# Performance work log

Measured on AMD Instinct MI355X. Metric: run time of the kernel, lower is better.

Reference implementation:

```python
import jax, jax.numpy as jnp
import numpy as np

B, T, D, NH = 2, 2048, 1024, 16


def setup_inputs() -> dict:
    key = jax.random.key(0)
    ks = jax.random.split(key, 9)
    s = 0.02
    return {
        "x": jax.random.normal(ks[0], (B, T, D), jnp.float32),
        "Wq": jax.random.normal(ks[1], (D, D), jnp.float32) * s,
        "bq": jax.random.normal(ks[2], (D,), jnp.float32) * s,
        "Wk": jax.random.normal(ks[3], (D, D), jnp.float32) * s,
        "bk": jax.random.normal(ks[4], (D,), jnp.float32) * s,
        "Wv": jax.random.normal(ks[5], (D, D), jnp.float32) * s,
        "bv": jax.random.normal(ks[6], (D,), jnp.float32) * s,
        "Wp": jax.random.normal(ks[7], (D, D), jnp.float32) * s,
        "bp": jax.random.normal(ks[8], (D,), jnp.float32) * s,
        "num_heads": NH,
    }


def _alibi_slopes(nh):
    # standard ALiBi slopes: 2^(-8*h/nh), h = 1..nh
    return jnp.asarray(2.0 ** (-8.0 * np.arange(1, nh + 1) / nh), jnp.float32)


def reference(x, Wq, bq, Wk, bk, Wv, bv, Wp, bp, num_heads):
    b, t, k = x.shape
    nh = num_heads
    hd = k // nh
    scale = k ** 0.25  # each of q,k divided by k**0.25 -> scores / sqrt(k)

    def split_heads(y):  # [b,t,k] -> [b,nh,t,hd]
        return y.reshape(b, t, nh, hd).transpose(0, 2, 1, 3)

    q = split_heads(x @ Wq.T + bq) / scale
    kk = split_heads(x @ Wk.T + bk) / scale
    v = split_heads(x @ Wv.T + bv)

    scores = jnp.einsum("bhid,bhjd->bhij", q, kk)  # [b,nh,t,t]

    pos = jnp.arange(t)
    rel = pos[None, :] - pos[:, None]  # j - i, <= 0 on causal side
    slopes = _alibi_slopes(nh)
    scores = scores + slopes[None, :, None, None] * rel[None, None, :, :]

    causal = rel <= 0  # [t,t]
    scores = jnp.where(causal[None, None, :, :], scores, -jnp.inf)

    attn = jax.nn.softmax(scores, axis=-1)
    out = jnp.einsum("bhij,bhjd->bhid", attn, v)  # [b,nh,t,hd]
    out = out.transpose(0, 2, 1, 3).reshape(b, t, k)
    return out @ Wp.T + bp
```

## Files before the change

kernel.cpp:

```cpp
#include <hip/hip_runtime.h>


using f32x4  = __attribute__((ext_vector_type(4))) float;
using bf16x8 = __attribute__((ext_vector_type(8))) short;
typedef unsigned short u16;
using u16x4 = __attribute__((ext_vector_type(4))) u16;
using u32x4 = __attribute__((ext_vector_type(4))) unsigned int;

#define T_SEQ  2048
#define NHEAD  16
#define HDIM   64
#define DMODEL 1024
#define MROWS  4096

#define LOG2E 1.4426950408889634f

__device__ __forceinline__ u16 f2bf(float f) {
  union { float f; unsigned u; } v; v.f = f;
  return (u16)((v.u + 0x7fffu + ((v.u >> 16) & 1u)) >> 16);
}

__device__ __forceinline__ unsigned cvt_pk_bf16(float lo, float hi) {
  unsigned r;
  asm("v_cvt_pk_bf16_f32 %0, %1, %2" : "=v"(r) : "v"(lo), "v"(hi));
  return r;
}

__device__ __forceinline__ void gl_lds16(const u16* g, u16* l) {
  __builtin_amdgcn_global_load_lds(
      (const __attribute__((address_space(1))) unsigned int*)g,
      (__attribute__((address_space(3))) unsigned int*)l, 16, 0, 0);
}

__global__ __launch_bounds__(256) void cvt_bf16(const float* __restrict__ src,
                                                u16* __restrict__ dst, int n) {
  int i = (blockIdx.x * 256 + threadIdx.x) * 4;
  if (i < n) {
    const float4 v = *reinterpret_cast<const float4*>(src + i);
    u16x4 o;
    o.x = f2bf(v.x); o.y = f2bf(v.y); o.z = f2bf(v.z); o.w = f2bf(v.w);
    *reinterpret_cast<u16x4*>(dst + i) = o;
  }
}

__global__ __launch_bounds__(256) void cvt_w4(
    const float* __restrict__ w0, const float* __restrict__ w1,
    const float* __restrict__ w2, const float* __restrict__ w3,
    u16* __restrict__ dst) {
  const float* src = (blockIdx.y == 0) ? w0 : (blockIdx.y == 1) ? w1
                   : (blockIdx.y == 2) ? w2 : w3;
  u16* d = dst + (size_t)blockIdx.y * 1048576;
  int i = (blockIdx.x * 256 + threadIdx.x) * 4;
  const float4 v = *reinterpret_cast<const float4*>(src + i);
  u16x4 o;
  o.x = f2bf(v.x); o.y = f2bf(v.y); o.z = f2bf(v.z); o.w = f2bf(v.w);
  *reinterpret_cast<u16x4*>(d + i) = o;
}

__global__ __launch_bounds__(256, 3) void qkv_gemm(
    const u16* __restrict__ xb,
    const u16* __restrict__ wq, const u16* __restrict__ wk, const u16* __restrict__ wv,
    const float* __restrict__ bq, const float* __restrict__ bk, const float* __restrict__ bv,
    u16* __restrict__ q_ws, u16* __restrict__ k_ws, u16* __restrict__ vt_ws)
{
  const int K = DMODEL;
  const int z = blockIdx.z;
  const u16*   W    = (z == 0) ? wq : (z == 1) ? wk : wv;
  const float* bias = (z == 0) ? bq : (z == 1) ? bk : bv;
  const int bm = blockIdx.y, bn = blockIdx.x;
  const int tid = threadIdx.x;
  const int w = tid >> 6, lane = tid & 63, g = lane >> 4, c = lane & 15;
  const int wm = w >> 1, wn = w & 1;

  __shared__ u16 SM[2][2][128][32];

  f32x4 zero4 = {0.f, 0.f, 0.f, 0.f};
  f32x4 acc[4][4];
#pragma unroll
  for (int m = 0; m < 4; ++m)
#pragma unroll
    for (int n = 0; n < 4; ++n) acc[m][n] = zero4;

  int rr[2], cswz[2];
#pragma unroll
  for (int jj = 0; jj < 2; ++jj) {
    int chunk = tid + 256 * jj;
    rr[jj] = chunk >> 2;
    cswz[jj] = ((chunk & 3) ^ (rr[jj] & 3)) * 8;
  }

  const int fsw = (g ^ (c & 3)) * 8;

#pragma unroll
  for (int jj = 0; jj < 2; ++jj) {
    int chunk = tid + 256 * jj;
    gl_lds16(xb + (size_t)(bm * 128 + rr[jj]) * K + cswz[jj],
             &SM[0][0][0][0] + chunk * 8);
    gl_lds16(W + (size_t)(bn * 128 + rr[jj]) * K + cswz[jj],
             &SM[0][1][0][0] + chunk * 8);
  }
  __syncthreads();

  for (int t = 0; t < 32; ++t) {
    const int buf = t & 1;
    if (t < 31) {
      const int k0 = (t + 1) * 32;
#pragma unroll
      for (int jj = 0; jj < 2; ++jj) {
        int chunk = tid + 256 * jj;
        gl_lds16(xb + (size_t)(bm * 128 + rr[jj]) * K + k0 + cswz[jj],
                 &SM[buf ^ 1][0][0][0] + chunk * 8);
        gl_lds16(W + (size_t)(bn * 128 + rr[jj]) * K + k0 + cswz[jj],
                 &SM[buf ^ 1][1][0][0] + chunk * 8);
      }
    }
    bf16x8 af[4], bfr[4];
#pragma unroll
    for (int m = 0; m < 4; ++m) {
      int row = wm * 64 + m * 16 + c;
      af[m] = *reinterpret_cast<const bf16x8*>(&SM[buf][0][row][fsw]);
    }
#pragma unroll
    for (int n = 0; n < 4; ++n) {
      int row = wn * 64 + n * 16 + c;
      bfr[n] = *reinterpret_cast<const bf16x8*>(&SM[buf][1][row][fsw]);
    }
#pragma unroll
    for (int m = 0; m < 4; ++m)
#pragma unroll
      for (int n = 0; n < 4; ++n)
        acc[m][n] = __builtin_amdgcn_mfma_f32_16x16x32_bf16(af[m], bfr[n], acc[m][n], 0, 0, 0);
    __syncthreads();
  }

  const float rs = 0.1767766953f;
  const float qs = rs * LOG2E;

  if (z == 2) {
    u16* tr = &SM[0][0][0][0];
    const int bb = (bm * 128) >> 11;
    const int t_base = (bm * 128) & (T_SEQ - 1);
#pragma unroll
    for (int hh = 0; hh < 2; ++hh) {
      __syncthreads();
      if (wn == hh) {
#pragma unroll
        for (int n = 0; n < 4; ++n) {
          float bv_ = bias[bn * 128 + wn * 64 + n * 16 + c];
#pragma unroll
          for (int m = 0; m < 4; ++m) {
#pragma unroll
            for (int i = 0; i < 4; ++i) {
              tr[(n * 16 + c) * 136 + wm * 64 + m * 16 + g * 4 + i] =
                  f2bf(acc[m][n][i] + bv_);
            }
          }
        }
      }
      __syncthreads();
#pragma unroll
      for (int rep = 0; rep < 4; ++rep) {
        int idx = tid + rep * 256;
        int dr = idx >> 4, ch = idx & 15;
        bf16x8 vv = *reinterpret_cast<const bf16x8*>(&tr[dr * 136 + ch * 8]);
        int d_glob = bn * 128 + hh * 64 + dr;
        int head = d_glob >> 6, dd = d_glob & 63;
        *reinterpret_cast<bf16x8*>(
            vt_ws + (((size_t)(bb * NHEAD + head) * HDIM + dd) * T_SEQ) + t_base + ch * 8) = vv;
      }
    }
  } else {
    u16* dst = (z == 0) ? q_ws : k_ws;
    const float sc = (z == 0) ? qs : rs;
#pragma unroll
    for (int m = 0; m < 4; ++m) {
      int mrow_base = bm * 128 + wm * 64 + m * 16 + g * 4;
#pragma unroll
      for (int n = 0; n < 4; ++n) {
        int n_idx = bn * 128 + wn * 64 + n * 16 + c;
        float bv_ = bias[n_idx];
        int head = n_idx >> 6, d = n_idx & 63;
#pragma unroll
        for (int i = 0; i < 4; ++i) {
          int mrow = mrow_base + i;
          int b = mrow >> 11, t = mrow & (T_SEQ - 1);
          dst[((size_t)(b * NHEAD + head) * T_SEQ + t) * HDIM + d] =
              f2bf((acc[m][n][i] + bv_) * sc);
        }
      }
    }
  }
}

__global__ __launch_bounds__(128, 2) void attn_fused(
    const u16* __restrict__ Q, const u16* __restrict__ Kk,
    const u16* __restrict__ VT, u16* __restrict__ O)
{
  const int tid = threadIdx.x;
  const int w = tid >> 6;
  const int lane = tid & 63;
  const int g = lane >> 4, c = lane & 15;
  const int c7 = c & 7;
  const int bid = blockIdx.x;
  const int inner = bid >> 3;
  const int bh = (bid & 7) + 8 * (inner & 3);
  const int j = inner >> 2;
  const int h = bh & (NHEAD - 1), b = bh >> 4;
  const float slope2 = exp2f(-0.5f * (float)(h + 1)) * LOG2E;
  const u16* Qp = Q  + (size_t)bh * T_SEQ * HDIM;
  const u16* Kp = Kk + (size_t)bh * T_SEQ * HDIM;
  const u16* Vp = VT + (size_t)bh * HDIM * T_SEQ;

  __shared__ u16 KB[2][64][64];
  __shared__ u16 VB[2][64][64];

  const int s_rb = tid >> 3;
  const int cs = ((tid & 7) ^ (s_rb & 7)) * 8;
  const u16* KsB = Kp + (size_t)s_rb * HDIM + cs;
  const u16* VsB = Vp + (size_t)s_rb * T_SEQ + cs;
  u16* const kd0 = &KB[0][0][0] + tid * 8;
  u16* const vd0 = &VB[0][0][0] + tid * 8;
  const int koffA = c * 64 + ((g ^ c7) * 8);
  const int koffB = c * 64 + (((4 + g) ^ c7) * 8);
  const int vre = c * 64 + (g & 1) * 4;
  const int voff0 = vre + ((((g >> 1) + 0) ^ c7) * 8);
  const int voff1 = vre + ((((g >> 1) + 2) ^ c7) * 8);
  const int voff2 = vre + ((((g >> 1) + 4) ^ c7) * 8);
  const int voff3 = vre + ((((g >> 1) + 6) ^ c7) * 8);

  f32x4 zero4 = {0.f, 0.f, 0.f, 0.f};

  for (int pass = 0; pass < 2; ++pass) {
    const int qb = (pass == 0) ? (63 - j) : j;
    const int q0 = qb * 32;
    const int qrow = q0 + w * 16;
    const int nt = (qb >> 1) + 1;

    bf16x8 qf0 = *reinterpret_cast<const bf16x8*>(Qp + (size_t)(qrow + c) * HDIM + g * 8);
    bf16x8 qf1 = *reinterpret_cast<const bf16x8*>(Qp + (size_t)(qrow + c) * HDIM + 32 + g * 8);

    {
      const int kv0 = (nt - 1) * 64;
      const u16* ks = KsB + kv0 * 64;
      const u16* vs = VsB + kv0;
      gl_lds16(ks,         kd0);
      gl_lds16(ks + 1024,  kd0 + 1024);
      gl_lds16(ks + 2048,  kd0 + 2048);
      gl_lds16(ks + 3072,  kd0 + 3072);
      gl_lds16(vs,          vd0);
      gl_lds16(vs + 32768,  vd0 + 1024);
      gl_lds16(vs + 65536,  vd0 + 2048);
      gl_lds16(vs + 98304,  vd0 + 3072);
    }
    __syncthreads();

    f32x4 o[4];
#pragma unroll
    for (int dg = 0; dg < 4; ++dg) o[dg] = zero4;
    float lrun = 0.f;

    for (int t = 0; t < nt; ++t) {
      const int par = t & 1;
      const u16* kb = &KB[0][0][0] + par * 4096;
      const u16* vb = &VB[0][0][0] + par * 4096;

      if (t + 1 < nt) {
        const int kvn = (nt - 2 - t) * 64;
        const u16* ks = KsB + kvn * 64;
        const u16* vs = VsB + kvn;
        u16* kd = kd0 + (par ^ 1) * 4096;
        u16* vd = vd0 + (par ^ 1) * 4096;
        gl_lds16(ks,         kd);
        gl_lds16(ks + 1024,  kd + 1024);
        gl_lds16(ks + 2048,  kd + 2048);
        gl_lds16(ks + 3072,  kd + 3072);
        gl_lds16(vs,          vd);
        gl_lds16(vs + 32768,  vd + 1024);
        gl_lds16(vs + 65536,  vd + 2048);
        gl_lds16(vs + 98304,  vd + 3072);
      }

      const int kv0 = (nt - 1 - t) * 64;

      const u16* kA = kb + koffA;
      const u16* kBp = kb + koffB;
      f32x4 s[4];
#pragma unroll
      for (int jj = 0; jj < 4; ++jj) {
        bf16x8 k0 = *reinterpret_cast<const bf16x8*>(kA + jj * 1024);
        bf16x8 k1 = *reinterpret_cast<const bf16x8*>(kBp + jj * 1024);
        f32x4 z4 = zero4;
        z4 = __builtin_amdgcn_mfma_f32_16x16x32_bf16(k0, qf0, z4, 0, 0, 0);
        z4 = __builtin_amdgcn_mfma_f32_16x16x32_bf16(k1, qf1, z4, 0, 0, 0);
        s[jj] = z4;
      }

      const int kbase = kv0 + 4 * g - (qrow + c);
      float p[16];
      if (t == 0) {
#pragma unroll
        for (int jj = 0; jj < 4; ++jj)
#pragma unroll
          for (int i = 0; i < 4; ++i) {
            int rel = kbase + 16 * jj + i;
            float sv = s[jj][i] + slope2 * (float)rel;
            if (rel > 0) sv = -3.0e38f;
            float e = __builtin_amdgcn_exp2f(sv);
            p[jj * 4 + i] = e;
            lrun += e;
          }
      } else {
        const float bb2 = slope2 * (float)kbase;
#pragma unroll
        for (int jj = 0; jj < 4; ++jj)
#pragma unroll
          for (int i = 0; i < 4; ++i) {
            float e = __builtin_amdgcn_exp2f(
                s[jj][i] + (bb2 + slope2 * (float)(16 * jj + i)));
            p[jj * 4 + i] = e;
            lrun += e;
          }
      }
      union PU { bf16x8 v; u32x4 u; };
      PU P0, P1;
#pragma unroll
      for (int k = 0; k < 4; ++k) {
        P0.u[k] = cvt_pk_bf16(p[2 * k], p[2 * k + 1]);
        P1.u[k] = cvt_pk_bf16(p[8 + 2 * k], p[8 + 2 * k + 1]);
      }

      const u16* vp0 = vb + voff0;
      const u16* vp1 = vb + voff1;
      const u16* vp2 = vb + voff2;
      const u16* vp3 = vb + voff3;
#pragma unroll
      for (int dg = 0; dg < 4; ++dg) {
        uint2 d0 = *reinterpret_cast<const uint2*>(vp0 + dg * 1024);
        uint2 d1 = *reinterpret_cast<const uint2*>(vp1 + dg * 1024);
        uint2 d2 = *reinterpret_cast<const uint2*>(vp2 + dg * 1024);
        uint2 d3 = *reinterpret_cast<const uint2*>(vp3 + dg * 1024);
        PU vf0, vf1;
        vf0.u[0] = d0.x; vf0.u[1] = d0.y; vf0.u[2] = d1.x; vf0.u[3] = d1.y;
        vf1.u[0] = d2.x; vf1.u[1] = d2.y; vf1.u[2] = d3.x; vf1.u[3] = d3.y;
        o[dg] = __builtin_amdgcn_mfma_f32_16x16x32_bf16(P0.v, vf0.v, o[dg], 0, 0, 0);
        o[dg] = __builtin_amdgcn_mfma_f32_16x16x32_bf16(P1.v, vf1.v, o[dg], 0, 0, 0);
      }

      __syncthreads();
    }

    lrun += __shfl_xor(lrun, 16, 64);
    lrun += __shfl_xor(lrun, 32, 64);
    float rl[4];
#pragma unroll
    for (int i = 0; i < 4; ++i) {
      float li = __shfl(lrun, g * 4 + i, 64);
      rl[i] = 1.0f / li;
    }
#pragma unroll
    for (int dg = 0; dg < 4; ++dg) {
#pragma unroll
      for (int i = 0; i < 4; ++i) {
        int qi = qrow + g * 4 + i;
        O[((size_t)b * T_SEQ + qi) * DMODEL + h * HDIM + dg * 16 + c] =
            f2bf(o[dg][i] * rl[i]);
      }
    }
    __syncthreads();
  }
}

__global__ __launch_bounds__(256) void out_gemm(
    const u16* __restrict__ ao, const u16* __restrict__ wp,
    const float* __restrict__ bp, float* __restrict__ out)
{
  const int K = DMODEL;
  const int bm = blockIdx.y, bn = blockIdx.x;
  const int tid = threadIdx.x;
  const int w = tid >> 6, lane = tid & 63, g = lane >> 4, c = lane & 15;
  const int wm = w >> 1, wn = w & 1;

  __shared__ u16 SM[2][2][128][64];

  f32x4 zero4 = {0.f, 0.f, 0.f, 0.f};
  f32x4 acc[4][4];
#pragma unroll
  for (int m = 0; m < 4; ++m)
#pragma unroll
    for (int n = 0; n < 4; ++n) acc[m][n] = zero4;

  int rr[4], cswz[4];
#pragma unroll
  for (int j = 0; j < 4; ++j) {
    int chunk = tid + 256 * j;
    rr[j] = chunk >> 3;
    cswz[j] = ((chunk & 7) ^ (rr[j] & 7)) * 8;
  }

#pragma unroll
  for (int j = 0; j < 4; ++j) {
    int chunk = tid + 256 * j;
    gl_lds16(ao + (size_t)(bm * 128 + rr[j]) * K + cswz[j],
             &SM[0][0][0][0] + chunk * 8);
    gl_lds16(wp + (size_t)(bn * 128 + rr[j]) * K + cswz[j],
             &SM[0][1][0][0] + chunk * 8);
  }
  __syncthreads();

  for (int t = 0; t < 16; ++t) {
    const int buf = t & 1;
    if (t < 15) {
      const int k0 = (t + 1) * 64;
#pragma unroll
      for (int j = 0; j < 4; ++j) {
        int chunk = tid + 256 * j;
        gl_lds16(ao + (size_t)(bm * 128 + rr[j]) * K + k0 + cswz[j],
                 &SM[buf ^ 1][0][0][0] + chunk * 8);
        gl_lds16(wp + (size_t)(bn * 128 + rr[j]) * K + k0 + cswz[j],
                 &SM[buf ^ 1][1][0][0] + chunk * 8);
      }
    }
#pragma unroll
    for (int kk = 0; kk < 2; ++kk) {
      bf16x8 af[4], bfr[4];
#pragma unroll
      for (int m = 0; m < 4; ++m) {
        int row = wm * 64 + m * 16 + c;
        af[m] = *reinterpret_cast<const bf16x8*>(
            &SM[buf][0][row][(kk * 32 + g * 8) ^ ((row & 7) * 8)]);
      }
#pragma unroll
      for (int n = 0; n < 4; ++n) {
        int row = wn * 64 + n * 16 + c;
        bfr[n] = *reinterpret_cast<const bf16x8*>(
            &SM[buf][1][row][(kk * 32 + g * 8) ^ ((row & 7) * 8)]);
      }
#pragma unroll
      for (int m = 0; m < 4; ++m)
#pragma unroll
        for (int n = 0; n < 4; ++n)
          acc[m][n] = __builtin_amdgcn_mfma_f32_16x16x32_bf16(af[m], bfr[n], acc[m][n], 0, 0, 0);
    }
    __syncthreads();
  }

#pragma unroll
  for (int m = 0; m < 4; ++m) {
    int mrow_base = bm * 128 + wm * 64 + m * 16 + g * 4;
#pragma unroll
    for (int n = 0; n < 4; ++n) {
      int n_idx = bn * 128 + wn * 64 + n * 16 + c;
      float bv_ = bp[n_idx];
#pragma unroll
      for (int i = 0; i < 4; ++i) {
        int mrow = mrow_base + i;
        out[(size_t)mrow * DMODEL + n_idx] = acc[m][n][i] + bv_;
      }
    }
  }
}

extern "C" void kernel_launch(void* const* d_in, const int* in_sizes, int n_in,
                              void* d_out, int out_size, void* d_ws, size_t ws_size,
                              hipStream_t stream) {
  const float* x  = (const float*)d_in[0];
  const float* Wq = (const float*)d_in[1];
  const float* bq = (const float*)d_in[2];
  const float* Wk = (const float*)d_in[3];
  const float* bk = (const float*)d_in[4];
  const float* Wv = (const float*)d_in[5];
  const float* bv = (const float*)d_in[6];
  const float* Wp = (const float*)d_in[7];
  const float* bp = (const float*)d_in[8];
  float* out = (float*)d_out;

  u16* ws    = (u16*)d_ws;
  u16* xb    = ws;
  u16* wqb   = xb   + 4194304;
  u16* wkb   = wqb  + 1048576;
  u16* wvb   = wkb  + 1048576;
  u16* wpb   = wvb  + 1048576;
  u16* q_ws  = wpb  + 1048576;
  u16* k_ws  = q_ws + 4194304;
  u16* vt_ws = k_ws + 4194304;
  u16* ao    = vt_ws + 4194304;

  cvt_bf16<<<4096, 256, 0, stream>>>(x, xb, 4194304);
  cvt_w4<<<dim3(1024, 4), 256, 0, stream>>>(Wq, Wk, Wv, Wp, wqb);

  qkv_gemm<<<dim3(DMODEL / 128, MROWS / 128, 3), 256, 0, stream>>>(
      xb, wqb, wkb, wvb, bq, bk, bv, q_ws, k_ws, vt_ws);

  attn_fused<<<1024, 128, 0, stream>>>(q_ws, k_ws, vt_ws, ao);

  out_gemm<<<dim3(DMODEL / 128, MROWS / 128), 256, 0, stream>>>(ao, wpb, bp, out);
}
```

Baseline: 103.3 us.

## Process 64-row query blocks per attention CTA and halve out-GEMM M tile

```diff
diff --git a/kernel.cpp b/kernel.cpp
--- a/kernel.cpp
+++ b/kernel.cpp
@@ -88,7 +88,6 @@
     rr[jj] = chunk >> 2;
     cswz[jj] = ((chunk & 3) ^ (rr[jj] & 3)) * 8;
   }
-
   const int fsw = (g ^ (c & 3)) * 8;
 
 #pragma unroll
@@ -192,7 +191,7 @@
   }
 }
 
-__global__ __launch_bounds__(128, 2) void attn_fused(
+__global__ __launch_bounds__(128) void attn_fused(
     const u16* __restrict__ Q, const u16* __restrict__ Kk,
     const u16* __restrict__ VT, u16* __restrict__ O)
 {
@@ -204,7 +203,7 @@
   const int bid = blockIdx.x;
   const int inner = bid >> 3;
   const int bh = (bid & 7) + 8 * (inner & 3);
-  const int j = inner >> 2;
+  const int p = inner >> 2;
   const int h = bh & (NHEAD - 1), b = bh >> 4;
   const float slope2 = exp2f(-0.5f * (float)(h + 1)) * LOG2E;
   const u16* Qp = Q  + (size_t)bh * T_SEQ * HDIM;
@@ -231,18 +230,20 @@
   f32x4 zero4 = {0.f, 0.f, 0.f, 0.f};
 
   for (int pass = 0; pass < 2; ++pass) {
-    const int qb = (pass == 0) ? (63 - j) : j;
-    const int q0 = qb * 32;
-    const int qrow = q0 + w * 16;
-    const int nt = (qb >> 1) + 1;
-
-    bf16x8 qf0 = *reinterpret_cast<const bf16x8*>(Qp + (size_t)(qrow + c) * HDIM + g * 8);
-    bf16x8 qf1 = *reinterpret_cast<const bf16x8*>(Qp + (size_t)(qrow + c) * HDIM + 32 + g * 8);
+    const int qb = (pass == 0) ? (31 - p) : p;
+    const int q0 = qb * 64;
+    const int qrowA = q0 + w * 32;
+    const int qrowB = qrowA + 16;
+    const int nt = qb + 1;
+
+    bf16x8 qfA0 = *reinterpret_cast<const bf16x8*>(Qp + (size_t)(qrowA + c) * HDIM + g * 8);
+    bf16x8 qfA1 = *reinterpret_cast<const bf16x8*>(Qp + (size_t)(qrowA + c) * HDIM + 32 + g * 8);
+    bf16x8 qfB0 = *reinterpret_cast<const bf16x8*>(Qp + (size_t)(qrowB + c) * HDIM + g * 8);
+    bf16x8 qfB1 = *reinterpret_cast<const bf16x8*>(Qp + (size_t)(qrowB + c) * HDIM + 32 + g * 8);
 
     {
-      const int kv0 = (nt - 1) * 64;
-      const u16* ks = KsB + kv0 * 64;
-      const u16* vs = VsB + kv0;
+      const u16* ks = KsB + q0 * 64;
+      const u16* vs = VsB + q0;
       gl_lds16(ks,         kd0);
       gl_lds16(ks + 1024,  kd0 + 1024);
       gl_lds16(ks + 2048,  kd0 + 2048);
@@ -254,10 +255,10 @@
     }
     __syncthreads();
 
-    f32x4 o[4];
-#pragma unroll
-    for (int dg = 0; dg < 4; ++dg) o[dg] = zero4;
-    float lrun = 0.f;
+    f32x4 oA[4], oB[4];
+#pragma unroll
+    for (int dg = 0; dg < 4; ++dg) { oA[dg] = zero4; oB[dg] = zero4; }
+    float lrunA = 0.f, lrunB = 0.f;
 
     for (int t = 0; t < nt; ++t) {
       const int par = t & 1;
@@ -284,49 +285,67 @@
 
       const u16* kA = kb + koffA;
       const u16* kBp = kb + koffB;
-      f32x4 s[4];
+      f32x4 sA[4], sB[4];
 #pragma unroll
       for (int jj = 0; jj < 4; ++jj) {
         bf16x8 k0 = *reinterpret_cast<const bf16x8*>(kA + jj * 1024);
         bf16x8 k1 = *reinterpret_cast<const bf16x8*>(kBp + jj * 1024);
-        f32x4 z4 = zero4;
-        z4 = __builtin_amdgcn_mfma_f32_16x16x32_bf16(k0, qf0, z4, 0, 0, 0);
-        z4 = __builtin_amdgcn_mfma_f32_16x16x32_bf16(k1, qf1, z4, 0, 0, 0);
-        s[jj] = z4;
-      }
-
-      const int kbase = kv0 + 4 * g - (qrow + c);
-      float p[16];
+        f32x4 zA = zero4;
+        zA = __builtin_amdgcn_mfma_f32_16x16x32_bf16(k0, qfA0, zA, 0, 0, 0);
+        zA = __builtin_amdgcn_mfma_f32_16x16x32_bf16(k1, qfA1, zA, 0, 0, 0);
+        sA[jj] = zA;
+        f32x4 zB = zero4;
+        zB = __builtin_amdgcn_mfma_f32_16x16x32_bf16(k0, qfB0, zB, 0, 0, 0);
+        zB = __builtin_amdgcn_mfma_f32_16x16x32_bf16(k1, qfB1, zB, 0, 0, 0);
+        sB[jj] = zB;
+      }
+
+      const int kbA = kv0 + 4 * g - (qrowA + c);
+      const int kbB = kbA - 16;
+      float pA[16], pB[16];
       if (t == 0) {
 #pragma unroll
         for (int jj = 0; jj < 4; ++jj)
 #pragma unroll
           for (int i = 0; i < 4; ++i) {
-            int rel = kbase + 16 * jj + i;
-            float sv = s[jj][i] + slope2 * (float)rel;
-            if (rel > 0) sv = -3.0e38f;
-            float e = __builtin_amdgcn_exp2f(sv);
-            p[jj * 4 + i] = e;
-            lrun += e;
+            int relA = kbA + 16 * jj + i;
+            float svA = sA[jj][i] + slope2 * (float)relA;
+            if (relA > 0) svA = -3.0e38f;
+            float eA = __builtin_amdgcn_exp2f(svA);
+            pA[jj * 4 + i] = eA;
+            lrunA += eA;
+            int relB = kbB + 16 * jj + i;
+            float svB = sB[jj][i] + slope2 * (float)relB;
+            if (relB > 0) svB = -3.0e38f;
+            float eB = __builtin_amdgcn_exp2f(svB);
+            pB[jj * 4 + i] = eB;
+            lrunB += eB;
           }
       } else {
-        const float bb2 = slope2 * (float)kbase;
+        const float bbA = slope2 * (float)kbA;
+        const float bbB = slope2 * (float)kbB;
 #pragma unroll
         for (int jj = 0; jj < 4; ++jj)
 #pragma unroll
           for (int i = 0; i < 4; ++i) {
-            float e = __builtin_amdgcn_exp2f(
-                s[jj][i] + (bb2 + slope2 * (float)(16 * jj + i)));
-            p[jj * 4 + i] = e;
-            lrun += e;
+            float eA = __builtin_amdgcn_exp2f(
+                sA[jj][i] + (bbA + slope2 * (float)(16 * jj + i)));
+            pA[jj * 4 + i] = eA;
+            lrunA += eA;
+            float eB = __builtin_amdgcn_exp2f(
+                sB[jj][i] + (bbB + slope2 * (float)(16 * jj + i)));
+            pB[jj * 4 + i] = eB;
+            lrunB += eB;
           }
       }
       union PU { bf16x8 v; u32x4 u; };
-      PU P0, P1;
+      PU PA0, PA1, PB0, PB1;
 #pragma unroll
       for (int k = 0; k < 4; ++k) {
-        P0.u[k] = cvt_pk_bf16(p[2 * k], p[2 * k + 1]);
-        P1.u[k] = cvt_pk_bf16(p[8 + 2 * k], p[8 + 2 * k + 1]);
+        PA0.u[k] = cvt_pk_bf16(pA[2 * k], pA[2 * k + 1]);
+        PA1.u[k] = cvt_pk_bf16(pA[8 + 2 * k], pA[8 + 2 * k + 1]);
+        PB0.u[k] = cvt_pk_bf16(pB[2 * k], pB[2 * k + 1]);
+        PB1.u[k] = cvt_pk_bf16(pB[8 + 2 * k], pB[8 + 2 * k + 1]);
       }
 
       const u16* vp0 = vb + voff0;
@@ -342,28 +361,35 @@
         PU vf0, vf1;
         vf0.u[0] = d0.x; vf0.u[1] = d0.y; vf0.u[2] = d1.x; vf0.u[3] = d1.y;
         vf1.u[0] = d2.x; vf1.u[1] = d2.y; vf1.u[2] = d3.x; vf1.u[3] = d3.y;
-        o[dg] = __builtin_amdgcn_mfma_f32_16x16x32_bf16(P0.v, vf0.v, o[dg], 0, 0, 0);
-        o[dg] = __builtin_amdgcn_mfma_f32_16x16x32_bf16(P1.v, vf1.v, o[dg], 0, 0, 0);
+        oA[dg] = __builtin_amdgcn_mfma_f32_16x16x32_bf16(PA0.v, vf0.v, oA[dg], 0, 0, 0);
+        oA[dg] = __builtin_amdgcn_mfma_f32_16x16x32_bf16(PA1.v, vf1.v, oA[dg], 0, 0, 0);
+        oB[dg] = __builtin_amdgcn_mfma_f32_16x16x32_bf16(PB0.v, vf0.v, oB[dg], 0, 0, 0);
+        oB[dg] = __builtin_amdgcn_mfma_f32_16x16x32_bf16(PB1.v, vf1.v, oB[dg], 0, 0, 0);
       }
 
       __syncthreads();
     }
 
-    lrun += __shfl_xor(lrun, 16, 64);
-    lrun += __shfl_xor(lrun, 32, 64);
-    float rl[4];
+    lrunA += __shfl_xor(lrunA, 16, 64);
+    lrunA += __shfl_xor(lrunA, 32, 64);
+    lrunB += __shfl_xor(lrunB, 16, 64);
+    lrunB += __shfl_xor(lrunB, 32, 64);
+    float rlA[4], rlB[4];
 #pragma unroll
     for (int i = 0; i < 4; ++i) {
-      float li = __shfl(lrun, g * 4 + i, 64);
-      rl[i] = 1.0f / li;
+      rlA[i] = 1.0f / __shfl(lrunA, g * 4 + i, 64);
+      rlB[i] = 1.0f / __shfl(lrunB, g * 4 + i, 64);
     }
 #pragma unroll
     for (int dg = 0; dg < 4; ++dg) {
 #pragma unroll
       for (int i = 0; i < 4; ++i) {
-        int qi = qrow + g * 4 + i;
-        O[((size_t)b * T_SEQ + qi) * DMODEL + h * HDIM + dg * 16 + c] =
-            f2bf(o[dg][i] * rl[i]);
+        int qiA = qrowA + g * 4 + i;
+        int qiB = qrowB + g * 4 + i;
+        O[((size_t)b * T_SEQ + qiA) * DMODEL + h * HDIM + dg * 16 + c] =
+            f2bf(oA[dg][i] * rlA[i]);
+        O[((size_t)b * T_SEQ + qiB) * DMODEL + h * HDIM + dg * 16 + c] =
+            f2bf(oB[dg][i] * rlB[i]);
       }
     }
     __syncthreads();
@@ -380,30 +406,41 @@
   const int w = tid >> 6, lane = tid & 63, g = lane >> 4, c = lane & 15;
   const int wm = w >> 1, wn = w & 1;
 
-  __shared__ u16 SM[2][2][128][64];
+  __shared__ u16 SA[2][64][64];
+  __shared__ u16 SB[2][128][64];
 
   f32x4 zero4 = {0.f, 0.f, 0.f, 0.f};
-  f32x4 acc[4][4];
-#pragma unroll
-  for (int m = 0; m < 4; ++m)
+  f32x4 acc[2][4];
+#pragma unroll
+  for (int m = 0; m < 2; ++m)
 #pragma unroll
     for (int n = 0; n < 4; ++n) acc[m][n] = zero4;
 
-  int rr[4], cswz[4];
-#pragma unroll
-  for (int j = 0; j < 4; ++j) {
-    int chunk = tid + 256 * j;
-    rr[j] = chunk >> 3;
-    cswz[j] = ((chunk & 7) ^ (rr[j] & 7)) * 8;
-  }
-
-#pragma unroll
-  for (int j = 0; j < 4; ++j) {
-    int chunk = tid + 256 * j;
-    gl_lds16(ao + (size_t)(bm * 128 + rr[j]) * K + cswz[j],
-             &SM[0][0][0][0] + chunk * 8);
-    gl_lds16(wp + (size_t)(bn * 128 + rr[j]) * K + cswz[j],
-             &SM[0][1][0][0] + chunk * 8);
+  int rA[2], cA[2], rB[4], cB[4];
+#pragma unroll
+  for (int jj = 0; jj < 2; ++jj) {
+    int chunk = tid + 256 * jj;
+    rA[jj] = chunk >> 3;
+    cA[jj] = ((chunk & 7) ^ (rA[jj] & 7)) * 8;
+  }
+#pragma unroll
+  for (int jj = 0; jj < 4; ++jj) {
+    int chunk = tid + 256 * jj;
+    rB[jj] = chunk >> 3;
+    cB[jj] = ((chunk & 7) ^ (rB[jj] & 7)) * 8;
+  }
+
+#pragma unroll
+  for (int jj = 0; jj < 2; ++jj) {
+    int chunk = tid + 256 * jj;
+    gl_lds16(ao + (size_t)(bm * 64 + rA[jj]) * K + cA[jj],
+             &SA[0][0][0] + chunk * 8);
+  }
+#pragma unroll
+  for (int jj = 0; jj < 4; ++jj) {
+    int chunk = tid + 256 * jj;
+    gl_lds16(wp + (size_t)(bn * 128 + rB[jj]) * K + cB[jj],
+             &SB[0][0][0] + chunk * 8);
   }
   __syncthreads();
 
@@ -412,31 +449,35 @@
     if (t < 15) {
       const int k0 = (t + 1) * 64;
 #pragma unroll
-      for (int j = 0; j < 4; ++j) {
-        int chunk = tid + 256 * j;
-        gl_lds16(ao + (size_t)(bm * 128 + rr[j]) * K + k0 + cswz[j],
-                 &SM[buf ^ 1][0][0][0] + chunk * 8);
-        gl_lds16(wp + (size_t)(bn * 128 + rr[j]) * K + k0 + cswz[j],
-                 &SM[buf ^ 1][1][0][0] + chunk * 8);
+      for (int jj = 0; jj < 2; ++jj) {
+        int chunk = tid + 256 * jj;
+        gl_lds16(ao + (size_t)(bm * 64 + rA[jj]) * K + k0 + cA[jj],
+                 &SA[buf ^ 1][0][0] + chunk * 8);
+      }
+#pragma unroll
+      for (int jj = 0; jj < 4; ++jj) {
+        int chunk = tid + 256 * jj;
+        gl_lds16(wp + (size_t)(bn * 128 + rB[jj]) * K + k0 + cB[jj],
+                 &SB[buf ^ 1][0][0] + chunk * 8);
       }
     }
 #pragma unroll
     for (int kk = 0; kk < 2; ++kk) {
-      bf16x8 af[4], bfr[4];
-#pragma unroll
-      for (int m = 0; m < 4; ++m) {
-        int row = wm * 64 + m * 16 + c;
+      bf16x8 af[2], bfr[4];
+#pragma unroll
+      for (int m = 0; m < 2; ++m) {
+        int row = wm * 32 + m * 16 + c;
         af[m] = *reinterpret_cast<const bf16x8*>(
-            &SM[buf][0][row][(kk * 32 + g * 8) ^ ((row & 7) * 8)]);
+            &SA[buf][row][(kk * 32 + g * 8) ^ ((row & 7) * 8)]);
       }
 #pragma unroll
       for (int n = 0; n < 4; ++n) {
         int row = wn * 64 + n * 16 + c;
         bfr[n] = *reinterpret_cast<const bf16x8*>(
-            &SM[buf][1][row][(kk * 32 + g * 8) ^ ((row & 7) * 8)]);
-      }
-#pragma unroll
-      for (int m = 0; m < 4; ++m)
+            &SB[buf][row][(kk * 32 + g * 8) ^ ((row & 7) * 8)]);
+      }
+#pragma unroll
+      for (int m = 0; m < 2; ++m)
 #pragma unroll
         for (int n = 0; n < 4; ++n)
           acc[m][n] = __builtin_amdgcn_mfma_f32_16x16x32_bf16(af[m], bfr[n], acc[m][n], 0, 0, 0);
@@ -445,8 +486,8 @@
   }
 
 #pragma unroll
-  for (int m = 0; m < 4; ++m) {
-    int mrow_base = bm * 128 + wm * 64 + m * 16 + g * 4;
+  for (int m = 0; m < 2; ++m) {
+    int mrow_base = bm * 64 + wm * 32 + m * 16 + g * 4;
 #pragma unroll
     for (int n = 0; n < 4; ++n) {
       int n_idx = bn * 128 + wn * 64 + n * 16 + c;
@@ -491,7 +532,7 @@
   qkv_gemm<<<dim3(DMODEL / 128, MROWS / 128, 3), 256, 0, stream>>>(
       xb, wqb, wkb, wvb, bq, bk, bv, q_ws, k_ws, vt_ws);
 
-  attn_fused<<<1024, 128, 0, stream>>>(q_ws, k_ws, vt_ws, ao);
-
-  out_gemm<<<dim3(DMODEL / 128, MROWS / 128), 256, 0, stream>>>(ao, wpb, bp, out);
-}
+  attn_fused<<<512, 128, 0, stream>>>(q_ws, k_ws, vt_ws, ao);
+
+  out_gemm<<<dim3(DMODEL / 128, MROWS / 64), 256, 0, stream>>>(ao, wpb, bp, out);
+}
```

New measurement: 119.2 us. +15.4%, slower.
